# Kernel optimization log

Hardware: AMD Instinct MI355X
Metric: run time of the kernel (lower is better)

Reference implementation:

```python
import jax, jax.numpy as jnp
import numpy as np
from itertools import permutations

# Static problem sizes: L=5 qubits, q=2**(L+1)=64 features, |G|=5!=120, 20 actions
L = 5
Q = 2 ** (L + 1)          # 64
G = 120                   # 5!
HID = 128
NACT = 20
B, T = 32, 64


def _build_tables():
    perms = list(permutations(range(L)))
    pidx = {p: i for i, p in enumerate(perms)}
    # inverse_table[i] = index of p_i^{-1}
    inv = [pidx[tuple(np.argsort(p))] for p in perms]
    # cayley[i, j] = index of p_i * p_j  (perm_prod(pi,pj) = tuple(pi[k] for k in pj))
    cayley = np.array([[pidx[tuple(pi[k] for k in pj)] for pj in perms] for pi in perms])
    # Hm[u, g] = index of permutation u * g^{-1} applied to x for group term g
    Hm = cayley[:, inv]
    # Gmap[u, p] = g such that Hm[u, g] == p  (row-wise bijection)
    Gmap = np.empty_like(Hm)
    Gmap[np.arange(G)[:, None], Hm] = np.arange(G)[None, :]
    # feature-level index maps: x_permuted = x[..., featperm[p]] matches torch
    # reshape(b,t,2,..,2).permute(0,1,2, g+3).reshape
    base = np.arange(Q).reshape((2,) * (L + 1))
    featperm = np.stack([
        base.transpose((0,) + tuple(i + 1 for i in p)).reshape(-1) for p in perms
    ])
    # action cosets: action a=(q0,q1) collects all perms with (p[0],p[1])==a
    acts = list(permutations(range(L), 2))
    aidx = {a: i for i, a in enumerate(acts)}
    coset_id = np.array([aidx[(p[0], p[1])] for p in perms])
    coset_size = np.bincount(coset_id, minlength=len(acts)).astype(np.float32)
    return featperm, Gmap, coset_id, coset_size


FEATPERM, GMAP, COSET_ID, COSET_SIZE = _build_tables()


def setup_inputs() -> dict:
    key = jax.random.key(0)
    ks = jax.random.split(key, 7)
    s = (2.0 / HID) ** 0.5  # kaiming-ish scale
    return {
        "x": jax.random.normal(ks[0], (B, T, Q), jnp.float32),
        "eq_weight": jax.random.normal(ks[1], (G, Q, HID), jnp.float32) * s,
        "eq_bias": jax.random.uniform(ks[2], (G, HID), jnp.float32, -0.01, 0.01),
        "W1": jax.random.normal(ks[3], (HID, HID), jnp.float32) * s,
        "b1": jax.random.uniform(ks[4], (HID,), jnp.float32, -0.01, 0.01),
        "Wout": jax.random.normal(ks[5], (HID, NACT), jnp.float32) * s,
        "bout": jax.random.uniform(ks[6], (NACT,), jnp.float32, -0.01, 0.01),
    }


def reference(x, eq_weight, eq_bias, W1, b1, Wout, bout):
    featperm = jnp.asarray(FEATPERM)          # (G, Q) int
    gmap = jnp.asarray(GMAP)                  # (G, G) int
    coset_id = jnp.asarray(COSET_ID)          # (G,) int
    coset_size = jnp.asarray(COSET_SIZE)      # (NACT,) float

    # all qubit-level permutations of the input: (G, b, t, q)
    Xp = jnp.moveaxis(x[..., featperm], 2, 0)
    # Equivariant layer for ALL u at once:
    # result(u) = (1/G) * sum_p Xp[p] @ W[Gmap[u,p]] + mean_g bias[g]
    Wu = eq_weight[gmap]                      # (G_u, G_p, Q, HID)
    e = jnp.einsum('pbtq,upqh->ubth', Xp, Wu) / G + eq_bias.mean(0)
    h = jax.nn.relu(e)
    h = jax.nn.relu(h @ W1 + b1)              # second hidden layer (dropout_rate=0)
    out = h @ Wout + bout                     # (G, b, t, NACT)
    m = out.mean(-1)                          # (G, b, t)
    # y_i = mean over u in coset_i of m[u]
    y = jax.ops.segment_sum(m, coset_id, num_segments=NACT)
    y = y / coset_size[:, None, None]
    return jnp.transpose(y, (1, 2, 0))        # (b, t, NACT)
```

## Files before the change

### kernel.cpp

```cpp
#include <hip/hip_runtime.h>

typedef _Float16 f16;
typedef __attribute__((ext_vector_type(8))) _Float16 f16x8;
typedef __attribute__((ext_vector_type(4))) float f32x4;
typedef __attribute__((ext_vector_type(4))) unsigned int u32x4;
typedef __attribute__((ext_vector_type(8))) unsigned short ushort8;

#define QF   64
#define GG   120
#define HID  128
#define NACT 20
#define BTOT 2048

#define WEFF_OFF 0u
#define W1F_OFF  1966080u
#define MISC_OFF 1998848u
#define ABUF_OFF 1999936u

template <typename T>
__device__ __forceinline__ void keepv(T& v) { asm volatile("" : "+v"(v)); }

__device__ __forceinline__ unsigned idx_to_packed(int i) {
    unsigned avail = 0x43210u, pp = 0u;
    const int fct[4] = {24, 6, 2, 1};
#pragma unroll
    for (int k = 0; k < 4; ++k) {
        int d = i / fct[k]; i -= d * fct[k];
        pp |= ((avail >> (4 * d)) & 0xFu) << (4 * k);
        unsigned mask = (1u << (4 * d)) - 1u;
        avail = (avail & mask) | ((avail >> 4) & ~mask);
    }
    pp |= (avail & 0xFu) << 16;
    return pp;
}

__device__ __forceinline__ int packed_to_idx(unsigned pp) {
    const int fct[4] = {24, 6, 2, 1};
    int idx = 0;
#pragma unroll
    for (int k = 0; k < 4; ++k) {
        unsigned pk = (pp >> (4 * k)) & 0xFu;
        int c = 0;
#pragma unroll
        for (int j = k + 1; j < 5; ++j)
            c += (int)(((pp >> (4 * j)) & 0xFu) < pk);
        idx += c * fct[k];
    }
    return idx;
}

__device__ __forceinline__ unsigned compose_packed(unsigned pa, unsigned pb) {
    unsigned pc = 0;
#pragma unroll
    for (int k = 0; k < 5; ++k) {
        unsigned bk = (pb >> (4 * k)) & 0xFu;
        pc |= ((pa >> (4 * bk)) & 0xFu) << (4 * k);
    }
    return pc;
}

__device__ __forceinline__ unsigned invert_packed(unsigned pp) {
    unsigned pi = 0;
#pragma unroll
    for (int k = 0; k < 5; ++k)
        pi |= (unsigned)k << (4 * ((pp >> (4 * k)) & 0xFu));
    return pi;
}

__device__ __forceinline__ unsigned s4_packed(int i) {
    unsigned avail = 0x3210u, pp = 0u;
    const int f3[3] = {6, 2, 1};
#pragma unroll
    for (int k = 0; k < 3; ++k) {
        int d = i / f3[k]; i -= d * f3[k];
        pp |= ((avail >> (4 * d)) & 0xFu) << (4 * k);
        unsigned mask = (1u << (4 * d)) - 1u;
        avail = (avail & mask) | ((avail >> 4) & ~mask);
    }
    pp |= (avail & 0xFu) << 12;
    pp |= 4u << 16;
    return pp;
}

__device__ __forceinline__ unsigned crep_pp(int t) {
    unsigned pp = 0x43210u;
    pp &= ~(0xFu << (4 * t));
    pp &= ~(0xFu << 16);
    pp |= 4u << (4 * t);
    pp |= (unsigned)t << 16;
    return pp;
}

__device__ __forceinline__ int bitperm_r(unsigned ppi, int r) {
    int val = r & 32;
#pragma unroll
    for (int k = 0; k < 5; ++k) {
        int pik = (ppi >> (4 * k)) & 0xF;
        val |= ((r >> (4 - pik)) & 1) << (4 - k);
    }
    return val;
}

__device__ __forceinline__ int coset_member(int a, int e) {
    int i = a >> 2, jj = a & 3;
    int j = jj + (jj >= i ? 1 : 0);
    unsigned mask = 0x1Fu & ~(1u << i) & ~(1u << j);
    int d0 = __builtin_ctz(mask); mask &= mask - 1u;
    int d1 = __builtin_ctz(mask); mask &= mask - 1u;
    int d2 = __builtin_ctz(mask);
    int k0 = e >> 1;
    int p2 = k0 == 0 ? d0 : (k0 == 1 ? d1 : d2);
    int r0 = k0 == 0 ? d1 : d0;
    int r1 = k0 == 2 ? d1 : d2;
    int p3 = (e & 1) ? r1 : r0;
    int p4 = (e & 1) ? r0 : r1;
    unsigned pp = (unsigned)i | ((unsigned)j << 4) | ((unsigned)p2 << 8)
                | ((unsigned)p3 << 12) | ((unsigned)p4 << 16);
    return packed_to_idx(pp);
}

__device__ __forceinline__ unsigned short f2h(float f) {
    f16 h = (f16)f;
    return __builtin_bit_cast(unsigned short, h);
}
__device__ __forceinline__ unsigned pk2(float a, float b) {
    return (unsigned)f2h(a) | ((unsigned)f2h(b) << 16);
}

__device__ __forceinline__ f32x4 mfma16(f16x8 a, f16x8 b, f32x4 c) {
    return __builtin_amdgcn_mfma_f32_16x16x32_f16(a, b, c, 0, 0, 0);
}

__global__ void k1_acanon(const float* __restrict__ eqw, float* __restrict__ Acan) {
    __shared__ int sg[24];
    __shared__ int sq[24][8];
    int b = blockIdx.x, t = threadIdx.x;
    int c = b >> 3, rbase = (b & 7) * 8;
    if (t < 24) sg[t] = packed_to_idx(compose_packed(s4_packed(t), crep_pp(c)));
    if (t < 192) {
        int si = t >> 3;
        sq[si][t & 7] = bitperm_r(invert_packed(s4_packed(si)), rbase + (t & 7));
    }
    __syncthreads();
    int h4 = (t & 31) * 4, rslot = t >> 5;
    f32x4 acc = {0.f, 0.f, 0.f, 0.f};
#pragma unroll
    for (int si = 0; si < 24; ++si) {
        f32x4 v = *(const f32x4*)(eqw + (unsigned)(sg[si] * QF + sq[si][rslot]) * HID + h4);
        acc = acc + v;
    }
    *(f32x4*)(Acan + (unsigned)(c * QF + rbase + rslot) * HID + h4) = acc;
}

__global__ void k2_weff(const float* __restrict__ Acan, const float* __restrict__ W1,
                        const float* __restrict__ eq_bias, const float* __restrict__ Wout,
                        const float* __restrict__ bout,
                        unsigned short* __restrict__ weff,
                        unsigned short* __restrict__ w1f, float* __restrict__ misc) {
    __shared__ float Wacc[HID][QF + 1];
    __shared__ int rp[5][64];
    int b = blockIdx.x, t = threadIdx.x;
    if (b < 120) {
        int u = b;
        unsigned upk = idx_to_packed(u);
        for (int i = t; i < 5 * 64; i += 256)
            rp[i >> 6][i & 63] = bitperm_r(compose_packed(upk, crep_pp(i >> 6)), i & 63);
        __syncthreads();
        int h = t & 127, qg = t >> 7;
        for (int i = 0; i < 32; ++i) {
            int q = qg * 32 + i;
            float s = 0.f;
#pragma unroll
            for (int c = 0; c < 5; ++c)
                s += Acan[(unsigned)(c * QF + rp[c][q]) * HID + h];
            Wacc[h][q] = s * (1.f / GG);
        }
        __syncthreads();
        for (int e = t; e < 1024; e += 256) {
            int fg = e >> 6, lane = e & 63;
            int hm = fg >> 1, ks = fg & 1;
            int hh = hm * 16 + (lane & 15), q0 = ks * 32 + (lane >> 4) * 8;
            ushort8 v;
#pragma unroll
            for (int j = 0; j < 8; ++j) v[j] = f2h(Wacc[hh][q0 + j]);
            *(ushort8*)(weff + (unsigned)(u * 16 + fg) * 64 * 8 + lane * 8) = v;
        }
    } else if (b < 128) {
        int idx = (b - 120) * 256 + t;
        int fg = idx >> 6, lane = idx & 63;
        int nt = fg >> 2, ks = fg & 3;
        int n = nt * 16 + (lane & 15), kg = lane >> 4;
        ushort8 v;
#pragma unroll
        for (int j = 0; j < 8; ++j) {
            int h = ks * 32 + ((j >> 2) << 4) + (kg << 2) + (j & 3);
            v[j] = f2h(W1[h * HID + n]);
        }
        *(ushort8*)(w1f + idx * 8) = v;
    } else {
        if (t < HID) {
            float s = 0.f;
            for (int g = 0; g < GG; ++g) s += eq_bias[g * HID + t];
            misc[t] = s * (1.f / GG);
            float wv = 0.f;
            for (int n = 0; n < NACT; ++n) wv += Wout[t * NACT + n];
            misc[HID + t] = wv * (1.f / NACT);
            if (t == 0) {
                float c = 0.f;
                for (int n = 0; n < NACT; ++n) c += bout[n];
                misc[2 * HID] = c * (1.f / NACT);
            }
        }
    }
}

__global__ __launch_bounds__(128, 2)
void mlp_mfma(const float* __restrict__ x,
              const unsigned short* __restrict__ weff,
              const unsigned short* __restrict__ w1f,
              const float* __restrict__ b1,
              const float* __restrict__ misc,
              float* __restrict__ out) {
    __shared__ __align__(16) unsigned short w1s[16384];
    __shared__ __align__(16) unsigned short wefs[8192];
    __shared__ float miscs[2 * HID];
    __shared__ float b1s[HID];

    int bid0 = blockIdx.x;
    int bid = (bid0 & 7) * 80 + (bid0 >> 3);
    int tile = bid & 31, a = bid >> 5;
    int rowbase = tile * 64;
    int t = threadIdx.x;
    int w = t >> 6, lane = t & 63;
    int lm = lane & 15, kg = lane >> 4;
    int xbase = rowbase + w * 32;

    int u0 = coset_member(a, 0);
#pragma unroll
    for (int i = 0; i < 16; ++i)
        *(u32x4*)(w1s + (i * 128 + t) * 8) = *(const u32x4*)(w1f + (i * 128 + t) * 8);
#pragma unroll
    for (int i = 0; i < 8; ++i)
        *(u32x4*)(wefs + (i * 128 + t) * 8) =
            *(const u32x4*)(weff + (unsigned)u0 * 8192 + (i * 128 + t) * 8);
    miscs[t] = misc[t];
    miscs[128 + t] = misc[128 + t];
    b1s[t] = b1[t];
    float cb = misc[2 * HID];

    f16x8 xb[2][2];
#pragma unroll
    for (int xt = 0; xt < 2; ++xt)
#pragma unroll
        for (int ks = 0; ks < 2; ++ks) {
            const float* xp = x + (unsigned)(xbase + xt * 16 + lm) * QF + ks * 32 + kg * 8;
            f32x4 a0 = *(const f32x4*)xp;
            f32x4 a1 = *(const f32x4*)(xp + 4);
            ushort8 v;
            v[0] = f2h(a0[0]); v[1] = f2h(a0[1]); v[2] = f2h(a0[2]); v[3] = f2h(a0[3]);
            v[4] = f2h(a1[0]); v[5] = f2h(a1[1]); v[6] = f2h(a1[2]); v[7] = f2h(a1[3]);
            xb[xt][ks] = __builtin_bit_cast(f16x8, v);
            keepv(xb[xt][ks]);
        }
    __syncthreads();

    float macc[2][4];
#pragma unroll
    for (int xt = 0; xt < 2; ++xt)
#pragma unroll
        for (int r = 0; r < 4; ++r) macc[xt][r] = 0.f;

#pragma unroll 1
    for (int ui = 0; ui < 6; ++ui) {
        bool hasNext = (ui < 5);
        u32x4 pf[8];
        if (hasNext) {
            int un = coset_member(a, ui + 1);
            const unsigned short* wsrc = weff + (unsigned)un * 8192;
#pragma unroll
            for (int i = 0; i < 8; ++i)
                pf[i] = *(const u32x4*)(wsrc + (i * 128 + t) * 8);
        }

        f32x4 acc[2][8];
#pragma unroll
        for (int xt = 0; xt < 2; ++xt)
#pragma unroll
            for (int hm = 0; hm < 8; ++hm) acc[xt][hm] = (f32x4){0.f, 0.f, 0.f, 0.f};
#pragma unroll
        for (int hm = 0; hm < 8; ++hm)
#pragma unroll
            for (int ks = 0; ks < 2; ++ks) {
                f16x8 wf = *(const f16x8*)(wefs + ((hm * 2 + ks) * 64 + lane) * 8);
#pragma unroll
                for (int xt = 0; xt < 2; ++xt)
                    acc[xt][hm] = mfma16(wf, xb[xt][ks], acc[xt][hm]);
            }

        __syncthreads();
        if (hasNext) {
#pragma unroll
            for (int i = 0; i < 8; ++i)
                *(u32x4*)(wefs + (i * 128 + t) * 8) = pf[i];
        }

        f32x4 acc2[2][8];
#pragma unroll
        for (int xt = 0; xt < 2; ++xt)
#pragma unroll
            for (int nt = 0; nt < 8; ++nt) acc2[xt][nt] = (f32x4){0.f, 0.f, 0.f, 0.f};
#pragma unroll
        for (int ks = 0; ks < 4; ++ks) {
            f32x4 bm0 = *(const f32x4*)(miscs + (2 * ks) * 16 + kg * 4);
            f32x4 bm1 = *(const f32x4*)(miscs + (2 * ks + 1) * 16 + kg * 4);
            f16x8 pa[2];
#pragma unroll
            for (int xt = 0; xt < 2; ++xt) {
                f32x4 e0 = acc[xt][2 * ks] + bm0;
                f32x4 e1 = acc[xt][2 * ks + 1] + bm1;
#pragma unroll
                for (int r = 0; r < 4; ++r) {
                    e0[r] = e0[r] > 0.f ? e0[r] : 0.f;
                    e1[r] = e1[r] > 0.f ? e1[r] : 0.f;
                }
                u32x4 ph = {pk2(e0[0], e0[1]), pk2(e0[2], e0[3]),
                            pk2(e1[0], e1[1]), pk2(e1[2], e1[3])};
                pa[xt] = __builtin_bit_cast(f16x8, ph);
            }
#pragma unroll
            for (int nt = 0; nt < 8; ++nt) {
                f16x8 wb = *(const f16x8*)(w1s + ((nt * 4 + ks) * 64 + lane) * 8);
#pragma unroll
                for (int xt = 0; xt < 2; ++xt)
                    acc2[xt][nt] = mfma16(pa[xt], wb, acc2[xt][nt]);
            }
        }

#pragma unroll
        for (int nt = 0; nt < 8; ++nt) {
            float bb = b1s[nt * 16 + lm];
            float wm = miscs[HID + nt * 16 + lm];
#pragma unroll
            for (int xt = 0; xt < 2; ++xt)
#pragma unroll
                for (int r = 0; r < 4; ++r) {
                    float v = acc2[xt][nt][r] + bb;
                    v = v > 0.f ? v : 0.f;
                    macc[xt][r] += v * wm;
                }
        }
        __syncthreads();
    }

#pragma unroll
    for (int off = 1; off < 16; off <<= 1)
#pragma unroll
        for (int xt = 0; xt < 2; ++xt)
#pragma unroll
            for (int r = 0; r < 4; ++r)
                macc[xt][r] += __shfl_xor(macc[xt][r], off, 64);
    if (lm == 0) {
#pragma unroll
        for (int xt = 0; xt < 2; ++xt)
#pragma unroll
            for (int r = 0; r < 4; ++r)
                out[(unsigned)(xbase + xt * 16 + kg * 4 + r) * NACT + a] =
                    macc[xt][r] * (1.f / 6.f) + cb;
    }
}

extern "C" void kernel_launch(void* const* d_in, const int* in_sizes, int n_in,
                              void* d_out, int out_size, void* d_ws, size_t ws_size,
                              hipStream_t stream) {
    const float* x       = (const float*)d_in[0];
    const float* eqw     = (const float*)d_in[1];
    const float* eq_bias = (const float*)d_in[2];
    const float* W1      = (const float*)d_in[3];
    const float* b1      = (const float*)d_in[4];
    const float* Wout    = (const float*)d_in[5];
    const float* bout    = (const float*)d_in[6];
    float* out           = (float*)d_out;

    char* ws = (char*)d_ws;
    unsigned short* weff = (unsigned short*)(ws + WEFF_OFF);
    unsigned short* w1f  = (unsigned short*)(ws + W1F_OFF);
    float* misc   = (float*)(ws + MISC_OFF);
    float* Acan   = (float*)(ws + ABUF_OFF);

    hipLaunchKernelGGL(k1_acanon, dim3(40), dim3(256), 0, stream, eqw, Acan);
    hipLaunchKernelGGL(k2_weff, dim3(129), dim3(256), 0, stream,
                       Acan, W1, eq_bias, Wout, bout, weff, w1f, misc);
    hipLaunchKernelGGL(mlp_mfma, dim3(640), dim3(128), 0, stream,
                       x, weff, w1f, b1, misc, out);
}
```

Measured before the change: 41.96 us.

## Load equivariant weights directly from global into registers, drop LDS staging and barriers

Removes the shared-memory double-buffer for the per-member equivariant weight tile. Each wave now reads its MFMA fragments straight from global memory (L2-resident) in two halves. The first GEMM is split so each half feeds the second GEMM immediately, which lowers live accumulator registers. This drops both __syncthreads per iteration and frees LDS, possibly allowing more blocks per CU. In exchange, the global load latency is no longer hidden by explicit prefetch, and both waves load the same data redundantly.

```diff
diff --git a/kernel.cpp b/kernel.cpp
--- a/kernel.cpp
+++ b/kernel.cpp
@@ -222,7 +222,6 @@
               const float* __restrict__ misc,
               float* __restrict__ out) {
     __shared__ __align__(16) unsigned short w1s[16384];
-    __shared__ __align__(16) unsigned short wefs[8192];
     __shared__ float miscs[2 * HID];
     __shared__ float b1s[HID];
 
@@ -235,14 +234,9 @@
     int lm = lane & 15, kg = lane >> 4;
     int xbase = rowbase + w * 32;
 
-    int u0 = coset_member(a, 0);
 #pragma unroll
     for (int i = 0; i < 16; ++i)
         *(u32x4*)(w1s + (i * 128 + t) * 8) = *(const u32x4*)(w1f + (i * 128 + t) * 8);
-#pragma unroll
-    for (int i = 0; i < 8; ++i)
-        *(u32x4*)(wefs + (i * 128 + t) * 8) =
-            *(const u32x4*)(weff + (unsigned)u0 * 8192 + (i * 128 + t) * 8);
     miscs[t] = misc[t];
     miscs[128 + t] = misc[128 + t];
     b1s[t] = b1[t];
@@ -272,67 +266,62 @@
 
 #pragma unroll 1
     for (int ui = 0; ui < 6; ++ui) {
-        bool hasNext = (ui < 5);
-        u32x4 pf[8];
-        if (hasNext) {
-            int un = coset_member(a, ui + 1);
-            const unsigned short* wsrc = weff + (unsigned)un * 8192;
-#pragma unroll
-            for (int i = 0; i < 8; ++i)
-                pf[i] = *(const u32x4*)(wsrc + (i * 128 + t) * 8);
-        }
-
-        f32x4 acc[2][8];
+        int u = coset_member(a, ui);
+        const unsigned short* wsrc = weff + (unsigned)u * 8192;
+
+        f32x4 acc2[2][8];
 #pragma unroll
         for (int xt = 0; xt < 2; ++xt)
 #pragma unroll
-            for (int hm = 0; hm < 8; ++hm) acc[xt][hm] = (f32x4){0.f, 0.f, 0.f, 0.f};
-#pragma unroll
-        for (int hm = 0; hm < 8; ++hm)
-#pragma unroll
-            for (int ks = 0; ks < 2; ++ks) {
-                f16x8 wf = *(const f16x8*)(wefs + ((hm * 2 + ks) * 64 + lane) * 8);
-#pragma unroll
-                for (int xt = 0; xt < 2; ++xt)
-                    acc[xt][hm] = mfma16(wf, xb[xt][ks], acc[xt][hm]);
-            }
-
-        __syncthreads();
-        if (hasNext) {
-#pragma unroll
-            for (int i = 0; i < 8; ++i)
-                *(u32x4*)(wefs + (i * 128 + t) * 8) = pf[i];
-        }
-
-        f32x4 acc2[2][8];
-#pragma unroll
-        for (int xt = 0; xt < 2; ++xt)
-#pragma unroll
             for (int nt = 0; nt < 8; ++nt) acc2[xt][nt] = (f32x4){0.f, 0.f, 0.f, 0.f};
-#pragma unroll
-        for (int ks = 0; ks < 4; ++ks) {
-            f32x4 bm0 = *(const f32x4*)(miscs + (2 * ks) * 16 + kg * 4);
-            f32x4 bm1 = *(const f32x4*)(miscs + (2 * ks + 1) * 16 + kg * 4);
-            f16x8 pa[2];
-#pragma unroll
-            for (int xt = 0; xt < 2; ++xt) {
-                f32x4 e0 = acc[xt][2 * ks] + bm0;
-                f32x4 e1 = acc[xt][2 * ks + 1] + bm1;
-#pragma unroll
-                for (int r = 0; r < 4; ++r) {
-                    e0[r] = e0[r] > 0.f ? e0[r] : 0.f;
-                    e1[r] = e1[r] > 0.f ? e1[r] : 0.f;
+
+#pragma unroll
+        for (int half = 0; half < 2; ++half) {
+            f16x8 wfr[8];
+#pragma unroll
+            for (int f = 0; f < 8; ++f)
+                wfr[f] = *(const f16x8*)(wsrc + ((half * 8 + f) * 64 + lane) * 8);
+
+            f32x4 acc[2][4];
+#pragma unroll
+            for (int xt = 0; xt < 2; ++xt)
+#pragma unroll
+                for (int hl = 0; hl < 4; ++hl) acc[xt][hl] = (f32x4){0.f, 0.f, 0.f, 0.f};
+#pragma unroll
+            for (int hl = 0; hl < 4; ++hl)
+#pragma unroll
+                for (int ks = 0; ks < 2; ++ks)
+#pragma unroll
+                    for (int xt = 0; xt < 2; ++xt)
+                        acc[xt][hl] = mfma16(wfr[hl * 2 + ks], xb[xt][ks], acc[xt][hl]);
+
+#pragma unroll
+            for (int ksl = 0; ksl < 2; ++ksl) {
+                int ksp = 2 * half + ksl;
+                int hg0 = 4 * half + 2 * ksl;
+                f32x4 bm0 = *(const f32x4*)(miscs + hg0 * 16 + kg * 4);
+                f32x4 bm1 = *(const f32x4*)(miscs + (hg0 + 1) * 16 + kg * 4);
+                f16x8 pa[2];
+#pragma unroll
+                for (int xt = 0; xt < 2; ++xt) {
+                    f32x4 e0 = acc[xt][2 * ksl] + bm0;
+                    f32x4 e1 = acc[xt][2 * ksl + 1] + bm1;
+#pragma unroll
+                    for (int r = 0; r < 4; ++r) {
+                        e0[r] = e0[r] > 0.f ? e0[r] : 0.f;
+                        e1[r] = e1[r] > 0.f ? e1[r] : 0.f;
+                    }
+                    u32x4 ph = {pk2(e0[0], e0[1]), pk2(e0[2], e0[3]),
+                                pk2(e1[0], e1[1]), pk2(e1[2], e1[3])};
+                    pa[xt] = __builtin_bit_cast(f16x8, ph);
                 }
-                u32x4 ph = {pk2(e0[0], e0[1]), pk2(e0[2], e0[3]),
-                            pk2(e1[0], e1[1]), pk2(e1[2], e1[3])};
-                pa[xt] = __builtin_bit_cast(f16x8, ph);
-            }
-#pragma unroll
-            for (int nt = 0; nt < 8; ++nt) {
-                f16x8 wb = *(const f16x8*)(w1s + ((nt * 4 + ks) * 64 + lane) * 8);
-#pragma unroll
-                for (int xt = 0; xt < 2; ++xt)
-                    acc2[xt][nt] = mfma16(pa[xt], wb, acc2[xt][nt]);
+#pragma unroll
+                for (int nt = 0; nt < 8; ++nt) {
+                    f16x8 wb = *(const f16x8*)(w1s + ((nt * 4 + ksp) * 64 + lane) * 8);
+#pragma unroll
+                    for (int xt = 0; xt < 2; ++xt)
+                        acc2[xt][nt] = mfma16(pa[xt], wb, acc2[xt][nt]);
+                }
             }
         }
 
@@ -349,7 +338,6 @@
                     macc[xt][r] += v * wm;
                 }
         }
-        __syncthreads();
     }
 
 #pragma unroll
```

Result: slower. 56.84 us (+35.5%).
